# Optimization experiments

Hardware: AMD Instinct MI355X
Metric: run time of the kernel (lower is better)

Reference implementation:

```python
import jax, jax.numpy as jnp
import numpy as np

B, M, K, E, V, HOPS = 256, 128, 4, 512, 32000, 3


def setup_inputs() -> dict:
    key = jax.random.key(0)
    ks = jax.random.split(key, 12)

    def emb_table(k):
        t = 0.1 * jax.random.normal(k, (V, E), dtype=jnp.float32)
        return t.at[0].set(0.0)  # padding_idx=0

    inp = {
        "context": jax.random.randint(ks[0], (B, M, K), 0, V),
        "y_": jax.random.randint(ks[1], (B,), 0, V),
        "h_": jax.random.normal(ks[2], (1, B, E), dtype=jnp.float32),
        # embedding tables; C[i] tied to A[i+1], so distinct: A0,A1,A2,C2
        "A0": emb_table(ks[3]),
        "A1": emb_table(ks[4]),
        "A2": emb_table(ks[5]),
        "C2": emb_table(ks[6]),
        # GRU (single layer, single step): PyTorch layout [3E, E] and [3E]
        "W_ih": 0.05 * jax.random.normal(ks[7], (3 * E, E), dtype=jnp.float32),
        "W_hh": 0.05 * jax.random.normal(ks[8], (3 * E, E), dtype=jnp.float32),
        "b_ih": jnp.zeros((3 * E,), dtype=jnp.float32),
        "b_hh": jnp.zeros((3 * E,), dtype=jnp.float32),
        # lin_vocab: Linear(2E -> V)
        "lin_W": 0.02 * jax.random.normal(ks[9], (V, 2 * E), dtype=jnp.float32),
        "lin_b": jnp.zeros((V,), dtype=jnp.float32),
    }
    return inp


def _gru_step(x, h, W_ih, W_hh, b_ih, b_hh):
    gi = x @ W_ih.T + b_ih  # [B, 3E]
    gh = h @ W_hh.T + b_hh
    i_r, i_z, i_n = jnp.split(gi, 3, axis=-1)
    h_r, h_z, h_n = jnp.split(gh, 3, axis=-1)
    r = jax.nn.sigmoid(i_r + h_r)
    z = jax.nn.sigmoid(i_z + h_z)
    n = jnp.tanh(i_n + r * h_n)
    return (1.0 - z) * n + z * h


def reference(context, y_, h_, A0, A1, A2, C2, W_ih, W_hh, b_ih, b_hh, lin_W, lin_b):
    # memories[hop] = sum_k A[hop][context], memories[hops] = sum_k C[hops-1][context]
    tables = [A0, A1, A2, C2]
    memories = [t[context].sum(axis=2) for t in tables]  # each [B, M, E]

    m = A1[y_]  # C[0](y_) -- C[0].weight tied to A[1].weight, [B, E]
    h = _gru_step(m, h_[0], W_ih, W_hh, b_ih, b_hh)  # [B, E]

    q = h
    p = None
    p_vocab = None
    for hop in range(HOPS):
        p = jnp.einsum("bme,be->bm", memories[hop], q)  # dot-attention scores
        attn = jax.nn.softmax(p, axis=1)
        o = jnp.einsum("bm,bme->be", attn, memories[hop + 1])
        if hop == 0:
            p_vocab = jnp.concatenate([q, o], axis=1) @ lin_W.T + lin_b  # [B, V]
        q = q + o

    p_ptr = p  # last hop's pre-softmax scores [B, M]
    return (p_ptr, p_vocab, h[None])  # h: [1, B, E]
```

## Files before the change

### kernel.cpp

```cpp
#include <hip/hip_runtime.h>
#include <hip/hip_bf16.h>
#include <stdint.h>
#include <stddef.h>

#define Bb 256
#define Mm 128
#define Ee 512
#define Vv 32000
#define E3 1536

typedef __attribute__((ext_vector_type(8))) short bf16x8;
typedef __attribute__((ext_vector_type(4))) float f32x4;

__device__ __forceinline__ float bf2f(unsigned short u) {
  union { unsigned int i; float f; } v; v.i = ((unsigned int)u) << 16; return v.f;
}
__device__ __forceinline__ unsigned int f2bf(float f) {
  union { float f; unsigned int u; } v; v.f = f;
  unsigned int u = v.u;
  return ((u + 0x7fffu + ((u >> 16) & 1u)) >> 16);
}

#define IN2F_IDX(bb, col)                                                     \
  ((((size_t)((bb) >> 4) * 32 + ((col) >> 5)) * 512) +                        \
   (size_t)((((bb) & 15) + (((col) >> 3) & 3) * 16) * 8 + ((col) & 7)))

__global__ void convert_kernel(const float* __restrict__ A0, const float* __restrict__ A1,
                               const float* __restrict__ A2,
                               unsigned short* __restrict__ tabB) {
  const int t = blockIdx.y;
  const float* src = (t == 0) ? A0 : (t == 1) ? A1 : A2;
  unsigned short* dst = tabB + (size_t)t * Vv * Ee;
  const int n4 = Vv * Ee / 4;
  for (int i = blockIdx.x * blockDim.x + threadIdx.x; i < n4; i += gridDim.x * blockDim.x) {
    f32x4 v = __builtin_nontemporal_load((const f32x4*)src + i);
    unsigned int o0 = f2bf(v.x) | (f2bf(v.y) << 16);
    unsigned int o1 = f2bf(v.z) | (f2bf(v.w) << 16);
    ((uint2*)dst)[i] = make_uint2(o0, o1);
  }
}

__global__ void gru_gemm_kernel(const int* __restrict__ y,
                                const float* __restrict__ A1,
                                const float* __restrict__ hprev,
                                const float* __restrict__ W_ih,
                                const float* __restrict__ W_hh,
                                float* __restrict__ gi,
                                float* __restrict__ gh) {
  const int z = blockIdx.z;
  const float* W = z ? W_hh : W_ih;
  float* C = z ? gh : gi;
  const int by = blockIdx.x * 64;
  const int jy = blockIdx.y * 64;
  __shared__ float As[16][65];
  __shared__ float Bs[16][65];
  const int tx = threadIdx.x & 15, ty = threadIdx.x >> 4;
  float acc[4][4] = {};
  for (int k0 = 0; k0 < Ee; k0 += 16) {
#pragma unroll
    for (int it = 0; it < 4; ++it) {
      int r = ty + it * 16;
      int row = by + r;
      const float* arow = z ? (hprev + (size_t)row * Ee) : (A1 + (size_t)y[row] * Ee);
      As[tx][r] = arow[k0 + tx];
      Bs[tx][r] = W[(size_t)(jy + r) * Ee + k0 + tx];
    }
    __syncthreads();
#pragma unroll
    for (int kk = 0; kk < 16; ++kk) {
      float a[4], bb[4];
#pragma unroll
      for (int i = 0; i < 4; ++i) { a[i] = As[kk][ty * 4 + i]; bb[i] = Bs[kk][tx * 4 + i]; }
#pragma unroll
      for (int i = 0; i < 4; ++i)
#pragma unroll
        for (int j = 0; j < 4; ++j)
          acc[i][j] += a[i] * bb[j];
    }
    __syncthreads();
  }
#pragma unroll
  for (int i = 0; i < 4; ++i)
#pragma unroll
    for (int j = 0; j < 4; ++j)
      C[(size_t)(by + ty * 4 + i) * E3 + jy + tx * 4 + j] = acc[i][j];
}

__global__ __launch_bounds__(1024) void fused_kernel(
    const int* __restrict__ ctx,
    const unsigned short* __restrict__ tabB,
    const float* __restrict__ A0, const float* __restrict__ A1,
    const float* __restrict__ A2,
    const float* __restrict__ gi, const float* __restrict__ gh,
    const float* __restrict__ b_ih, const float* __restrict__ b_hh,
    const float* __restrict__ h0,
    float* __restrict__ out_h, unsigned short* __restrict__ in2f,
    float* __restrict__ p_out) {
  extern __shared__ char smem[];
  unsigned short* Vlds = (unsigned short*)smem;
  float* p_lds = (float*)(smem + 131072);
  float* qbuf = (float*)(smem + 131584);
  float* obuf = (float*)(smem + 133632);

  const int b = blockIdx.x;
  const int tid = threadIdx.x;
  const int lane = tid & 63, w = tid >> 6;

  if (tid < 512) {
    const int e = tid;
    const float* gib = gi + (size_t)b * E3;
    const float* ghb = gh + (size_t)b * E3;
    float ir = gib[e] + b_ih[e];
    float iz = gib[512 + e] + b_ih[512 + e];
    float inn = gib[1024 + e] + b_ih[1024 + e];
    float hr = ghb[e] + b_hh[e];
    float hz = ghb[512 + e] + b_hh[512 + e];
    float hn = ghb[1024 + e] + b_hh[1024 + e];
    float r = 1.f / (1.f + __expf(-(ir + hr)));
    float z = 1.f / (1.f + __expf(-(iz + hz)));
    float n = tanhf(inn + r * hn);
    float hp = h0[(size_t)b * Ee + e];
    float hnew = (1.f - z) * n + z * hp;
    out_h[(size_t)b * Ee + e] = hnew;
    in2f[IN2F_IDX(b, e)] = (unsigned short)f2bf(hnew);
    qbuf[e] = hnew;
  }

#define GATHER_B(T)                                                          \
  {                                                                          \
    const unsigned short* Tb = tabB + (size_t)(T) * ((size_t)Vv * Ee);       \
    _Pragma("unroll 2")                                                      \
    for (int r8 = 0; r8 < 8; ++r8) {                                         \
      const int row = w * 8 + r8;                                            \
      const int4 cc = *(const int4*)(ctx + ((size_t)b * Mm + row) * 4);      \
      uint4 va = *(const uint4*)(Tb + (size_t)cc.x * Ee + lane * 8);         \
      uint4 vb = *(const uint4*)(Tb + (size_t)cc.y * Ee + lane * 8);         \
      uint4 vc = *(const uint4*)(Tb + (size_t)cc.z * Ee + lane * 8);         \
      uint4 vd = *(const uint4*)(Tb + (size_t)cc.w * Ee + lane * 8);         \
      const unsigned int* pa = (const unsigned int*)&va;                     \
      const unsigned int* pb = (const unsigned int*)&vb;                     \
      const unsigned int* pc = (const unsigned int*)&vc;                     \
      const unsigned int* pd = (const unsigned int*)&vd;                     \
      unsigned int o[4];                                                     \
      _Pragma("unroll")                                                      \
      for (int j = 0; j < 4; ++j) {                                          \
        float lo = bf2f((unsigned short)(pa[j] & 0xffff)) +                  \
                   bf2f((unsigned short)(pb[j] & 0xffff)) +                  \
                   bf2f((unsigned short)(pc[j] & 0xffff)) +                  \
                   bf2f((unsigned short)(pd[j] & 0xffff));                   \
        float hi = bf2f((unsigned short)(pa[j] >> 16)) +                     \
                   bf2f((unsigned short)(pb[j] >> 16)) +                     \
                   bf2f((unsigned short)(pc[j] >> 16)) +                     \
                   bf2f((unsigned short)(pd[j] >> 16));                      \
        o[j] = f2bf(lo) | (f2bf(hi) << 16);                                  \
      }                                                                      \
      *(uint4*)(Vlds + (size_t)row * Ee + lane * 8) = *(uint4*)o;            \
    }                                                                        \
  }

#define GATHER_F(TAB)                                                        \
  {                                                                          \
    _Pragma("unroll 2")                                                      \
    for (int r8 = 0; r8 < 8; ++r8) {                                         \
      const int row = w * 8 + r8;                                            \
      const int4 cc = *(const int4*)(ctx + ((size_t)b * Mm + row) * 4);      \
      const float* s0 = TAB + (size_t)cc.x * Ee + lane * 8;                  \
      const float* s1 = TAB + (size_t)cc.y * Ee + lane * 8;                  \
      const float* s2 = TAB + (size_t)cc.z * Ee + lane * 8;                  \
      const float* s3 = TAB + (size_t)cc.w * Ee + lane * 8;                  \
      float4 a0 = *(const float4*)s0, a1 = *(const float4*)(s0 + 4);         \
      float4 b0 = *(const float4*)s1, b1 = *(const float4*)(s1 + 4);         \
      float4 c0 = *(const float4*)s2, c1 = *(const float4*)(s2 + 4);         \
      float4 d0 = *(const float4*)s3, d1 = *(const float4*)(s3 + 4);         \
      unsigned int o[4];                                                     \
      o[0] = f2bf(a0.x + b0.x + c0.x + d0.x) |                               \
             (f2bf(a0.y + b0.y + c0.y + d0.y) << 16);                        \
      o[1] = f2bf(a0.z + b0.z + c0.z + d0.z) |                               \
             (f2bf(a0.w + b0.w + c0.w + d0.w) << 16);                        \
      o[2] = f2bf(a1.x + b1.x + c1.x + d1.x) |                               \
             (f2bf(a1.y + b1.y + c1.y + d1.y) << 16);                        \
      o[3] = f2bf(a1.z + b1.z + c1.z + d1.z) |                               \
             (f2bf(a1.w + b1.w + c1.w + d1.w) << 16);                        \
      *(uint4*)(Vlds + (size_t)row * Ee + lane * 8) = *(uint4*)o;            \
    }                                                                        \
  }

#define GATHER(T, TAB) { if (tabB) GATHER_B(T) else GATHER_F(TAB) }

#define SCORE_PHASE(EMIT)                                                    \
  {                                                                          \
    float qf[8];                                                             \
    *(float4*)&qf[0] = *(const float4*)&qbuf[lane * 8];                      \
    *(float4*)&qf[4] = *(const float4*)&qbuf[lane * 8 + 4];                  \
    _Pragma("unroll")                                                        \
    for (int r = 0; r < 8; ++r) {                                            \
      const int m = w * 8 + r;                                               \
      uint4 kv = *(const uint4*)(Vlds + (size_t)m * Ee + lane * 8);          \
      const unsigned int* p4 = (const unsigned int*)&kv;                     \
      float s = 0.f;                                                         \
      _Pragma("unroll")                                                      \
      for (int x = 0; x < 4; ++x) {                                          \
        s += bf2f((unsigned short)(p4[x] & 0xffff)) * qf[2 * x];             \
        s += bf2f((unsigned short)(p4[x] >> 16)) * qf[2 * x + 1];            \
      }                                                                      \
      _Pragma("unroll")                                                      \
      for (int off = 32; off > 0; off >>= 1) s += __shfl_down(s, off);       \
      if (lane == 0) { EMIT; }                                               \
    }                                                                        \
  }

#define SOFTMAX_PHASE                                                        \
  if (tid < 64) {                                                            \
    float v0 = p_lds[tid], v1 = p_lds[tid + 64];                             \
    float mx = fmaxf(v0, v1);                                                \
    _Pragma("unroll")                                                        \
    for (int off = 32; off > 0; off >>= 1) mx = fmaxf(mx, __shfl_xor(mx, off)); \
    float e0 = __expf(v0 - mx), e1 = __expf(v1 - mx);                        \
    float s = e0 + e1;                                                       \
    _Pragma("unroll")                                                        \
    for (int off = 32; off > 0; off >>= 1) s += __shfl_xor(s, off);          \
    float inv = 1.f / s;                                                     \
    p_lds[tid] = e0 * inv;                                                   \
    p_lds[tid + 64] = e1 * inv;                                              \
  }

#define O_PHASE                                                              \
  {                                                                          \
    const int g = tid >> 8, t = tid & 255;                                   \
    const int e2 = t * 2;                                                    \
    float a0 = 0.f, a1 = 0.f;                                                \
    _Pragma("unroll 4")                                                      \
    for (int m = g * 32; m < g * 32 + 32; ++m) {                             \
      unsigned int vv = *(const unsigned int*)(Vlds + (size_t)m * Ee + e2);  \
      float ww = p_lds[m];                                                   \
      a0 += ww * bf2f((unsigned short)(vv & 0xffff));                        \
      a1 += ww * bf2f((unsigned short)(vv >> 16));                           \
    }                                                                        \
    obuf[g * 512 + e2] = a0;                                                 \
    obuf[g * 512 + e2 + 1] = a1;                                             \
  }

  GATHER(0, A0)
  __syncthreads();
  SCORE_PHASE(p_lds[m] = s)
  __syncthreads();
  SOFTMAX_PHASE
  GATHER(1, A1)
  __syncthreads();
  O_PHASE
  __syncthreads();
  if (tid < 512) {
    const int e = tid;
    float o = obuf[e] + obuf[512 + e] + obuf[1024 + e] + obuf[1536 + e];
    qbuf[e] = qbuf[e] + o;
    in2f[IN2F_IDX(b, 512 + e)] = (unsigned short)f2bf(o);
  }
  __syncthreads();

  SCORE_PHASE(p_lds[m] = s)
  __syncthreads();
  SOFTMAX_PHASE
  GATHER(2, A2)
  __syncthreads();
  O_PHASE
  __syncthreads();
  if (tid < 512) {
    const int e = tid;
    qbuf[e] = qbuf[e] + obuf[e] + obuf[512 + e] + obuf[1024 + e] + obuf[1536 + e];
  }
  __syncthreads();

  SCORE_PHASE(p_out[b * Mm + m] = s)
}

__global__ __launch_bounds__(512, 2) void pvocab_kernel(
    const unsigned short* __restrict__ in2f,
    const float* __restrict__ lin_W,
    const float* __restrict__ lin_b,
    float* __restrict__ out_pv) {
  __shared__ __align__(16) unsigned short Ws[2][64][64];

  const int v0 = blockIdx.x * 64;
  const int tid = threadIdx.x;
  const int lane = tid & 63, w = tid >> 6;
  const int l15 = lane & 15, lg = lane >> 4;
  const int wc = tid & 15, wrb = tid >> 4;

  f32x4 acc[2][4];
#pragma unroll
  for (int i = 0; i < 2; ++i)
#pragma unroll
    for (int j = 0; j < 4; ++j)
      acc[i][j] = (f32x4){0.f, 0.f, 0.f, 0.f};

  uint4 aA[4], aB[4];
  float4 wR[2];

  const unsigned short* a_base0 = in2f + ((size_t)(2 * w) * 32) * 512 + lane * 8;
  const unsigned short* a_base1 = in2f + ((size_t)(2 * w + 1) * 32) * 512 + lane * 8;

#define PV_A_LOAD(T, BUF)                                                    \
  {                                                                          \
    BUF[0] = *(const uint4*)(a_base0 + (size_t)(2 * (T)) * 512);             \
    BUF[1] = *(const uint4*)(a_base0 + (size_t)(2 * (T) + 1) * 512);         \
    BUF[2] = *(const uint4*)(a_base1 + (size_t)(2 * (T)) * 512);             \
    BUF[3] = *(const uint4*)(a_base1 + (size_t)(2 * (T) + 1) * 512);         \
  }

#define PV_W_LOAD(T)                                                         \
  {                                                                          \
    wR[0] = *(const float4*)(lin_W + (size_t)(v0 + wrb) * 1024 + (T) * 64 + wc * 4);      \
    wR[1] = *(const float4*)(lin_W + (size_t)(v0 + wrb + 32) * 1024 + (T) * 64 + wc * 4); \
  }

#define PV_W_WRITE(WWI)                                                      \
  {                                                                          \
    _Pragma("unroll")                                                        \
    for (int it = 0; it < 2; ++it) {                                         \
      int r = wrb + it * 32;                                                 \
      unsigned int o0 = f2bf(wR[it].x) | (f2bf(wR[it].y) << 16);             \
      unsigned int o1 = f2bf(wR[it].z) | (f2bf(wR[it].w) << 16);             \
      int u = wc >> 1, h = wc & 1;                                           \
      *(uint2*)(&Ws[WWI][r][((u + r) & 7) * 8 + h * 4]) = make_uint2(o0, o1); \
    }                                                                        \
  }

#define PV_MFMA(ABUF, RWI)                                                   \
  {                                                                          \
    _Pragma("unroll")                                                        \
    for (int kb = 0; kb < 2; ++kb) {                                         \
      const int cu = kb * 4 + lg;                                            \
      bf16x8 wf[4];                                                          \
      _Pragma("unroll")                                                      \
      for (int nf = 0; nf < 4; ++nf) {                                       \
        int row = nf * 16 + l15;                                             \
        wf[nf] = *(const bf16x8*)(&Ws[RWI][row][((cu + row) & 7) * 8]);      \
      }                                                                      \
      _Pragma("unroll")                                                      \
      for (int mb = 0; mb < 2; ++mb) {                                       \
        bf16x8 af = *(const bf16x8*)&ABUF[mb * 2 + kb];                      \
        _Pragma("unroll")                                                    \
        for (int nf = 0; nf < 4; ++nf)                                       \
          acc[mb][nf] = __builtin_amdgcn_mfma_f32_16x16x32_bf16(af, wf[nf], acc[mb][nf], 0, 0, 0); \
      }                                                                      \
    }                                                                        \
  }

#define PV_BARRIER                                                           \
  asm volatile("s_waitcnt lgkmcnt(0)" ::: "memory");                         \
  __builtin_amdgcn_sched_barrier(0);                                         \
  __builtin_amdgcn_s_barrier();

#define PV_ITER(T, ABUF, RWI, WWI)                                           \
  {                                                                          \
    if ((T) + 1 < 16) PV_W_LOAD((T) + 1)                                     \
    PV_MFMA(ABUF, RWI)                                                       \
    if ((T) + 2 < 16) PV_A_LOAD((T) + 2, ABUF)                               \
    if ((T) + 1 < 16) {                                                      \
      PV_W_WRITE(WWI)                                                        \
      PV_BARRIER                                                             \
    }                                                                        \
  }

  PV_A_LOAD(0, aA)
  PV_A_LOAD(1, aB)
  PV_W_LOAD(0)
  PV_W_WRITE(0)
  PV_BARRIER

  PV_ITER(0, aA, 0, 1)
  PV_ITER(1, aB, 1, 0)
  PV_ITER(2, aA, 0, 1)
  PV_ITER(3, aB, 1, 0)
  PV_ITER(4, aA, 0, 1)
  PV_ITER(5, aB, 1, 0)
  PV_ITER(6, aA, 0, 1)
  PV_ITER(7, aB, 1, 0)
  PV_ITER(8, aA, 0, 1)
  PV_ITER(9, aB, 1, 0)
  PV_ITER(10, aA, 0, 1)
  PV_ITER(11, aB, 1, 0)
  PV_ITER(12, aA, 0, 1)
  PV_ITER(13, aB, 1, 0)
  PV_ITER(14, aA, 0, 1)
  PV_ITER(15, aB, 1, 0)

  {
#pragma unroll
    for (int nf = 0; nf < 4; ++nf) {
      int v = v0 + nf * 16 + l15;
      float bias = lin_b[v];
#pragma unroll
      for (int mb = 0; mb < 2; ++mb) {
        int brow = (2 * w + mb) * 16 + lg * 4;
#pragma unroll
        for (int rr = 0; rr < 4; ++rr)
          out_pv[(size_t)(brow + rr) * Vv + v] = acc[mb][nf][rr] + bias;
      }
    }
  }
}

extern "C" void kernel_launch(void* const* d_in, const int* in_sizes, int n_in,
                              void* d_out, int out_size, void* d_ws, size_t ws_size,
                              hipStream_t stream) {
  const int* ctx = (const int*)d_in[0];
  const int* y = (const int*)d_in[1];
  const float* h0 = (const float*)d_in[2];
  const float* A0 = (const float*)d_in[3];
  const float* A1 = (const float*)d_in[4];
  const float* A2 = (const float*)d_in[5];
  const float* W_ih = (const float*)d_in[7];
  const float* W_hh = (const float*)d_in[8];
  const float* b_ih = (const float*)d_in[9];
  const float* b_hh = (const float*)d_in[10];
  const float* lin_W = (const float*)d_in[11];
  const float* lin_b = (const float*)d_in[12];

  const size_t tabBytes = (size_t)3 * Vv * Ee * 2;
  const size_t giBytes = (size_t)Bb * E3 * 4;
  const size_t in2Bytes = (size_t)Bb * 1024 * 2;
  const bool bf16path = ws_size >= tabBytes + 2 * giBytes + in2Bytes;

  char* ws = (char*)d_ws;
  size_t off = 0;
  unsigned short* tabB = nullptr;
  if (bf16path) { tabB = (unsigned short*)ws; off += tabBytes; }
  float* gi = (float*)(ws + off); off += giBytes;
  float* gh = (float*)(ws + off); off += giBytes;
  unsigned short* in2f = (unsigned short*)(ws + off);

  float* out = (float*)d_out;
  float* p_ptr = out;
  float* p_voc = out + Bb * Mm;
  float* out_h = out + Bb * Mm + (size_t)Bb * Vv;

  if (bf16path)
    convert_kernel<<<dim3(4096, 3), 256, 0, stream>>>(A0, A1, A2, tabB);
  gru_gemm_kernel<<<dim3(4, 24, 2), 256, 0, stream>>>(y, A1, h0, W_ih, W_hh, gi, gh);
  hipFuncSetAttribute((const void*)fused_kernel,
                      hipFuncAttributeMaxDynamicSharedMemorySize, 141824);
  fused_kernel<<<Bb, 1024, 141824, stream>>>(ctx, tabB, A0, A1, A2, gi, gh,
                                             b_ih, b_hh, h0, out_h, in2f, p_ptr);
  pvocab_kernel<<<Vv / 64, 512, 0, stream>>>(in2f, lin_W, lin_b, p_voc);
}
```

Baseline: 211.2 us.

## Double pvocab block threads, giving each wave one 16-row batch tile

Restructures the vocab projection kernel to launch 1024 threads per block, with each wave computing a single 16-row batch tile instead of two. Each thread loads one weight float4 instead of two, and accumulator and A-fragment register counts halve. The aim is more resident waves to hide the global-memory latency of streaming lin_W. The trade-off is twice the LDS weight-fragment reads per MFMA and a tighter launch-bound register budget.

```diff
diff --git a/kernel.cpp b/kernel.cpp
--- a/kernel.cpp
+++ b/kernel.cpp
@@ -273,7 +273,7 @@
   SCORE_PHASE(p_out[b * Mm + m] = s)
 }
 
-__global__ __launch_bounds__(512, 2) void pvocab_kernel(
+__global__ __launch_bounds__(1024, 8) void pvocab_kernel(
     const unsigned short* __restrict__ in2f,
     const float* __restrict__ lin_W,
     const float* __restrict__ lin_b,
@@ -286,43 +286,30 @@
   const int l15 = lane & 15, lg = lane >> 4;
   const int wc = tid & 15, wrb = tid >> 4;
 
-  f32x4 acc[2][4];
-#pragma unroll
-  for (int i = 0; i < 2; ++i)
-#pragma unroll
-    for (int j = 0; j < 4; ++j)
-      acc[i][j] = (f32x4){0.f, 0.f, 0.f, 0.f};
-
-  uint4 aA[4], aB[4];
-  float4 wR[2];
-
-  const unsigned short* a_base0 = in2f + ((size_t)(2 * w) * 32) * 512 + lane * 8;
-  const unsigned short* a_base1 = in2f + ((size_t)(2 * w + 1) * 32) * 512 + lane * 8;
+  f32x4 acc[4];
+#pragma unroll
+  for (int j = 0; j < 4; ++j) acc[j] = (f32x4){0.f, 0.f, 0.f, 0.f};
+
+  uint4 aA[2], aB[2];
+  float4 wR;
+
+  const unsigned short* a_base = in2f + ((size_t)w * 32) * 512 + lane * 8;
 
 #define PV_A_LOAD(T, BUF)                                                    \
   {                                                                          \
-    BUF[0] = *(const uint4*)(a_base0 + (size_t)(2 * (T)) * 512);             \
-    BUF[1] = *(const uint4*)(a_base0 + (size_t)(2 * (T) + 1) * 512);         \
-    BUF[2] = *(const uint4*)(a_base1 + (size_t)(2 * (T)) * 512);             \
-    BUF[3] = *(const uint4*)(a_base1 + (size_t)(2 * (T) + 1) * 512);         \
+    BUF[0] = *(const uint4*)(a_base + (size_t)(2 * (T)) * 512);              \
+    BUF[1] = *(const uint4*)(a_base + (size_t)(2 * (T) + 1) * 512);          \
   }
 
 #define PV_W_LOAD(T)                                                         \
-  {                                                                          \
-    wR[0] = *(const float4*)(lin_W + (size_t)(v0 + wrb) * 1024 + (T) * 64 + wc * 4);      \
-    wR[1] = *(const float4*)(lin_W + (size_t)(v0 + wrb + 32) * 1024 + (T) * 64 + wc * 4); \
-  }
+  wR = *(const float4*)(lin_W + (size_t)(v0 + wrb) * 1024 + (T) * 64 + wc * 4);
 
 #define PV_W_WRITE(WWI)                                                      \
   {                                                                          \
-    _Pragma("unroll")                                                        \
-    for (int it = 0; it < 2; ++it) {                                         \
-      int r = wrb + it * 32;                                                 \
-      unsigned int o0 = f2bf(wR[it].x) | (f2bf(wR[it].y) << 16);             \
-      unsigned int o1 = f2bf(wR[it].z) | (f2bf(wR[it].w) << 16);             \
-      int u = wc >> 1, h = wc & 1;                                           \
-      *(uint2*)(&Ws[WWI][r][((u + r) & 7) * 8 + h * 4]) = make_uint2(o0, o1); \
-    }                                                                        \
+    unsigned int o0 = f2bf(wR.x) | (f2bf(wR.y) << 16);                       \
+    unsigned int o1 = f2bf(wR.z) | (f2bf(wR.w) << 16);                       \
+    int u = wc >> 1, h = wc & 1;                                             \
+    *(uint2*)(&Ws[WWI][wrb][((u + wrb) & 7) * 8 + h * 4]) = make_uint2(o0, o1); \
   }
 
 #define PV_MFMA(ABUF, RWI)                                                   \
@@ -330,18 +317,12 @@
     _Pragma("unroll")                                                        \
     for (int kb = 0; kb < 2; ++kb) {                                         \
       const int cu = kb * 4 + lg;                                            \
-      bf16x8 wf[4];                                                          \
+      bf16x8 af = *(bf16x8*)&ABUF[kb];                                       \
       _Pragma("unroll")                                                      \
       for (int nf = 0; nf < 4; ++nf) {                                       \
         int row = nf * 16 + l15;                                             \
-        wf[nf] = *(const bf16x8*)(&Ws[RWI][row][((cu + row) & 7) * 8]);      \
-      }                                                                      \
-      _Pragma("unroll")                                                      \
-      for (int mb = 0; mb < 2; ++mb) {                                       \
-        bf16x8 af = *(const bf16x8*)&ABUF[mb * 2 + kb];                      \
-        _Pragma("unroll")                                                    \
-        for (int nf = 0; nf < 4; ++nf)                                       \
-          acc[mb][nf] = __builtin_amdgcn_mfma_f32_16x16x32_bf16(af, wf[nf], acc[mb][nf], 0, 0, 0); \
+        bf16x8 wf = *(const bf16x8*)(&Ws[RWI][row][((cu + row) & 7) * 8]);   \
+        acc[nf] = __builtin_amdgcn_mfma_f32_16x16x32_bf16(af, wf, acc[nf], 0, 0, 0); \
       }                                                                      \
     }                                                                        \
   }
@@ -390,13 +371,10 @@
     for (int nf = 0; nf < 4; ++nf) {
       int v = v0 + nf * 16 + l15;
       float bias = lin_b[v];
-#pragma unroll
-      for (int mb = 0; mb < 2; ++mb) {
-        int brow = (2 * w + mb) * 16 + lg * 4;
-#pragma unroll
-        for (int rr = 0; rr < 4; ++rr)
-          out_pv[(size_t)(brow + rr) * Vv + v] = acc[mb][nf][rr] + bias;
-      }
+      int brow = w * 16 + lg * 4;
+#pragma unroll
+      for (int rr = 0; rr < 4; ++rr)
+        out_pv[(size_t)(brow + rr) * Vv + v] = acc[nf][rr] + bias;
     }
   }
 }
@@ -442,5 +420,5 @@
                       hipFuncAttributeMaxDynamicSharedMemorySize, 141824);
   fused_kernel<<<Bb, 1024, 141824, stream>>>(ctx, tabB, A0, A1, A2, gi, gh,
                                              b_ih, b_hh, h0, out_h, in2f, p_ptr);
-  pvocab_kernel<<<Vv / 64, 512, 0, stream>>>(in2f, lin_W, lin_b, p_voc);
-}
+  pvocab_kernel<<<Vv / 64, 1024, 0, stream>>>(in2f, lin_W, lin_b, p_voc);
+}
```

After: 214.1 us. Within noise of the previous version (+1.4%).
